# Optimization experiments

Measured on AMD Instinct MI355X. Metric: run time of the kernel, lower is better.

## Reference

```python
import jax, jax.numpy as jnp
import numpy as np

B, S, E, D = 4, 2048, 2048, 2048  # batch, seq (<= kvq_dim), embedding_dim, kvq_dim


def setup_inputs() -> dict:
    key = jax.random.key(0)
    kx, kk, kq, kv = jax.random.split(key, 4)
    x = jax.random.normal(kx, (B, S, E), dtype=jnp.float32)
    # torch nn.Linear weights are [out_features, in_features]
    Wk = jax.random.normal(kk, (D, E), dtype=jnp.float32) * 0.02
    Wq = jax.random.normal(kq, (D, E), dtype=jnp.float32) * 0.02
    Wv = jax.random.normal(kv, (D, E), dtype=jnp.float32) * 0.02
    return {"x": x, "Wk": Wk, "Wq": Wq, "Wv": Wv}


def reference(x, Wk, Wq, Wv):
    # Projections (Linear without bias): y = x @ W^T
    K = jnp.einsum("bse,de->bsd", x, Wk)
    Q = jnp.einsum("bse,de->bsd", x, Wq)
    V = jnp.einsum("bse,de->bsd", x, Wv)
    seq = x.shape[1]
    scores = jnp.einsum("bqd,bkd->bqk", Q, K)  # [B, S, S]
    causal = jnp.triu(jnp.ones((seq, seq), dtype=bool), k=1)
    masked = jnp.where(causal[None, :, :], -jnp.inf, scores)
    scale = K.shape[-1] ** 0.5  # -inf / scale stays -inf, matching the torch order
    attn = jax.nn.softmax(masked / scale, axis=-1)
    # dropout: reference evaluated in eval mode (identity)
    return jnp.einsum("bqk,bkd->bqd", attn, V)
```

## Files before the change

### kernel.cpp

```cpp
#include <hip/hip_runtime.h>
#include <hip/hip_bf16.h>
#include <stdint.h>


typedef unsigned short u16;
typedef unsigned int u32;
typedef __bf16 bf16x8 __attribute__((ext_vector_type(8)));
typedef float floatx4 __attribute__((ext_vector_type(4)));

#define DEVI __device__ __forceinline__

constexpr int Bn = 4, Sn = 2048, En = 2048, Dn = 2048;
constexpr int BM = 128, BN = 128, BK = 64;

DEVI u16 f2b(float f) {
  union { float f; u32 u; } v; v.f = f;
  u32 r = v.u + 0x7FFFu + ((v.u >> 16) & 1u);
  return (u16)(r >> 16);
}

DEVI void cp16(const u16* g, u16* l) {
  __builtin_amdgcn_global_load_lds(
      (const __attribute__((address_space(1))) void*)g,
      (__attribute__((address_space(3))) void*)l, 16, 0, 0);
}

__global__ __launch_bounds__(256)
void cvt_kernel(const float* __restrict__ src, u16* __restrict__ dst, int n) {
  int i = (blockIdx.x * 256 + threadIdx.x) * 8;
  if (i >= n) return;
  float4 a = *(const float4*)&src[i];
  float4 b = *(const float4*)&src[i + 4];
  *(ushort4*)&dst[i]     = make_ushort4(f2b(a.x), f2b(a.y), f2b(a.z), f2b(a.w));
  *(ushort4*)&dst[i + 4] = make_ushort4(f2b(b.x), f2b(b.y), f2b(b.z), f2b(b.w));
}

DEVI void gemm_core(const u16* __restrict__ A, const u16* __restrict__ Bt,
                    int lda, int ldb, int m0, int n0, int kEnd,
                    u16* As, u16* Bs, floatx4 acc[4][4]) {
  const int tid = threadIdx.x;
  const int lane = tid & 63;
  const int wave = tid >> 6;
  const int wm = (wave >> 1) * 64;
  const int wn = (wave & 1) * 64;
  const int quad = lane >> 4;
  const int l16 = lane & 15;
  const int sw = l16 & 7;

  int srow[4], sgl[4], sdst[4];
#pragma unroll
  for (int u = 0; u < 4; ++u) {
    int c0 = wave * 256 + u * 64;
    int c = c0 + lane;
    srow[u] = c >> 3;
    sgl[u] = (c & 7) ^ (srow[u] & 7);
    sdst[u] = c0 * 8;
  }

  for (int k0 = 0; k0 < kEnd; k0 += BK) {
#pragma unroll
    for (int u = 0; u < 4; ++u) {
      cp16(&A[(size_t)(m0 + srow[u]) * lda + k0 + sgl[u] * 8], &As[sdst[u]]);
      cp16(&Bt[(size_t)(n0 + srow[u]) * ldb + k0 + sgl[u] * 8], &Bs[sdst[u]]);
    }
    __syncthreads();
#pragma unroll
    for (int s = 0; s < 2; ++s) {
      const int gcol = ((s * 4 + quad) ^ sw) * 8;
      bf16x8 af[4], bfr[4];
#pragma unroll
      for (int i = 0; i < 4; ++i)
        af[i] = *(const bf16x8*)&As[(wm + i * 16 + l16) * 64 + gcol];
#pragma unroll
      for (int j = 0; j < 4; ++j)
        bfr[j] = *(const bf16x8*)&Bs[(wn + j * 16 + l16) * 64 + gcol];
#pragma unroll
      for (int i = 0; i < 4; ++i)
#pragma unroll
        for (int j = 0; j < 4; ++j)
          acc[i][j] = __builtin_amdgcn_mfma_f32_16x16x32_bf16(af[i], bfr[j], acc[i][j], 0, 0, 0);
    }
    __syncthreads();
  }
}

__global__ __launch_bounds__(256, 2)
void proj_kernel(const u16* __restrict__ x, const u16* __restrict__ Wq,
                 const u16* __restrict__ Wk, const u16* __restrict__ Wv,
                 u16* __restrict__ Q, u16* __restrict__ K, u16* __restrict__ Vt) {
  __shared__ __align__(16) u16 As[BM * 64], Bs[BN * 64];
  const int z = blockIdx.z;
  const u16* W = (z == 0) ? Wq : (z == 1) ? Wk : Wv;
  const int m0 = blockIdx.y * BM, n0 = blockIdx.x * BN;
  floatx4 acc[4][4] = {};
  gemm_core(x, W, En, En, m0, n0, En, As, Bs, acc);

  const int lane = threadIdx.x & 63, wave = threadIdx.x >> 6;
  const int wm = (wave >> 1) * 64, wn = (wave & 1) * 64;
  const int quad = lane >> 4, l16 = lane & 15;

  if (z < 2) {
    u16* dst = (z == 0) ? Q : K;
#pragma unroll
    for (int i = 0; i < 4; ++i) {
      int t0 = m0 + wm + i * 16 + quad * 4;
#pragma unroll
      for (int j = 0; j < 4; ++j) {
        int gn = n0 + wn + j * 16 + l16;
#pragma unroll
        for (int r = 0; r < 4; ++r)
          dst[(size_t)(t0 + r) * Dn + gn] = f2b(acc[i][j][r]);
      }
    }
  } else {
#pragma unroll
    for (int i = 0; i < 4; ++i) {
      int t0 = m0 + wm + i * 16 + quad * 4;
      int b = t0 >> 11, s0 = t0 & (Sn - 1);
#pragma unroll
      for (int j = 0; j < 4; ++j) {
        int gn = n0 + wn + j * 16 + l16;
        *(ushort4*)&Vt[((size_t)b * Dn + gn) * Sn + s0] =
            make_ushort4(f2b(acc[i][j][0]), f2b(acc[i][j][1]),
                         f2b(acc[i][j][2]), f2b(acc[i][j][3]));
      }
    }
  }
}

__global__ __launch_bounds__(256, 2)
void scores_kernel(const u16* __restrict__ Q, const u16* __restrict__ K,
                   float* __restrict__ Sc) {
  const int b = blockIdx.z;
  const int m0 = blockIdx.y * BM, n0 = blockIdx.x * BN;
  float* C = Sc + (size_t)b * Sn * Sn;
  if (n0 > m0 + (BM - 1)) {
    for (int idx = threadIdx.x; idx < BM * BN; idx += 256) {
      int r = idx >> 7, c = idx & (BN - 1);
      C[(size_t)(m0 + r) * Sn + n0 + c] = -1e30f;
    }
    return;
  }
  __shared__ __align__(16) u16 As[BM * 64], Bs[BN * 64];
  floatx4 acc[4][4] = {};
  gemm_core(Q + (size_t)b * Sn * Dn, K + (size_t)b * Sn * Dn, Dn, Dn, m0, n0, Dn,
            As, Bs, acc);

  const float inv_scale = 0.022097086912079608f;
  const int lane = threadIdx.x & 63, wave = threadIdx.x >> 6;
  const int wm = (wave >> 1) * 64, wn = (wave & 1) * 64;
  const int quad = lane >> 4, l16 = lane & 15;
#pragma unroll
  for (int i = 0; i < 4; ++i) {
    int gm0 = m0 + wm + i * 16 + quad * 4;
#pragma unroll
    for (int j = 0; j < 4; ++j) {
      int gn = n0 + wn + j * 16 + l16;
#pragma unroll
      for (int r = 0; r < 4; ++r) {
        float v = acc[i][j][r] * inv_scale;
        if (gn > gm0 + r) v = -1e30f;
        C[(size_t)(gm0 + r) * Sn + gn] = v;
      }
    }
  }
}

__global__ __launch_bounds__(256)
void softmax_kernel(float* __restrict__ Sc) {
  float* sr = Sc + (size_t)blockIdx.x * Sn;
  const int t = threadIdx.x;
  float4 v0 = ((const float4*)sr)[t];
  float4 v1 = ((const float4*)sr)[t + 256];
  float m = fmaxf(fmaxf(fmaxf(v0.x, v0.y), fmaxf(v0.z, v0.w)),
                  fmaxf(fmaxf(v1.x, v1.y), fmaxf(v1.z, v1.w)));
#pragma unroll
  for (int off = 32; off; off >>= 1) m = fmaxf(m, __shfl_xor(m, off));
  __shared__ float redm[4], reds[4];
  if ((t & 63) == 0) redm[t >> 6] = m;
  __syncthreads();
  m = fmaxf(fmaxf(redm[0], redm[1]), fmaxf(redm[2], redm[3]));

  float e[8];
  e[0] = __expf(v0.x - m); e[1] = __expf(v0.y - m);
  e[2] = __expf(v0.z - m); e[3] = __expf(v0.w - m);
  e[4] = __expf(v1.x - m); e[5] = __expf(v1.y - m);
  e[6] = __expf(v1.z - m); e[7] = __expf(v1.w - m);
  float s = ((e[0] + e[1]) + (e[2] + e[3])) + ((e[4] + e[5]) + (e[6] + e[7]));
#pragma unroll
  for (int off = 32; off; off >>= 1) s += __shfl_xor(s, off);
  if ((t & 63) == 0) reds[t >> 6] = s;
  __syncthreads();
  s = (reds[0] + reds[1]) + (reds[2] + reds[3]);
  float inv = 1.0f / s;

  u16* ar = (u16*)sr;
  *(ushort4*)&ar[t * 4] =
      make_ushort4(f2b(e[0] * inv), f2b(e[1] * inv), f2b(e[2] * inv), f2b(e[3] * inv));
  *(ushort4*)&ar[(t + 256) * 4] =
      make_ushort4(f2b(e[4] * inv), f2b(e[5] * inv), f2b(e[6] * inv), f2b(e[7] * inv));
}

__global__ __launch_bounds__(256, 2)
void pv_kernel(const float* __restrict__ Sc, const u16* __restrict__ Vt,
               float* __restrict__ out) {
  const int b = blockIdx.z;
  const int m0 = blockIdx.y * BM, n0 = blockIdx.x * BN;
  __shared__ __align__(16) u16 As[BM * 64], Bs[BN * 64];
  floatx4 acc[4][4] = {};
  const u16* P = (const u16*)(Sc + (size_t)b * Sn * Sn);
  gemm_core(P, Vt + (size_t)b * Dn * Sn, 2 * Sn, Sn, m0, n0, m0 + BM, As, Bs, acc);

  const int lane = threadIdx.x & 63, wave = threadIdx.x >> 6;
  const int wm = (wave >> 1) * 64, wn = (wave & 1) * 64;
  const int quad = lane >> 4, l16 = lane & 15;
  float* ob = out + (size_t)b * Sn * Dn;
#pragma unroll
  for (int i = 0; i < 4; ++i) {
    int gm0 = m0 + wm + i * 16 + quad * 4;
#pragma unroll
    for (int j = 0; j < 4; ++j) {
      int gn = n0 + wn + j * 16 + l16;
#pragma unroll
      for (int r = 0; r < 4; ++r)
        ob[(size_t)(gm0 + r) * Dn + gn] = acc[i][j][r];
    }
  }
}

extern "C" void kernel_launch(void* const* d_in, const int* in_sizes, int n_in,
                              void* d_out, int out_size, void* d_ws, size_t ws_size,
                              hipStream_t stream) {
  const float* x  = (const float*)d_in[0];
  const float* Wk = (const float*)d_in[1];
  const float* Wq = (const float*)d_in[2];
  const float* Wv = (const float*)d_in[3];
  float* out = (float*)d_out;

  dim3 blk(256);
  const int nW = Dn * En;
  const size_t MiB = 1ull << 20;

  if (ws_size >= 184 * MiB) {
    u16* Wqb = (u16*)d_ws;
    u16* Wkb = Wqb + (size_t)nW;
    u16* Wvb = Wkb + (size_t)nW;
    u16* xb  = Wvb + (size_t)nW;
    u16* Kall = xb + (size_t)Bn * Sn * En;
    u16* Vtall = Kall + (size_t)Bn * Sn * Dn;
    float* Sc = (float*)(Vtall + (size_t)Bn * Dn * Sn);
    u16* Qall = (u16*)out;

    cvt_kernel<<<nW / 2048, blk, 0, stream>>>(Wq, Wqb, nW);
    cvt_kernel<<<nW / 2048, blk, 0, stream>>>(Wk, Wkb, nW);
    cvt_kernel<<<nW / 2048, blk, 0, stream>>>(Wv, Wvb, nW);
    cvt_kernel<<<(Bn * Sn * En) / 2048, blk, 0, stream>>>(x, xb, Bn * Sn * En);
    proj_kernel<<<dim3(Dn / BN, (Bn * Sn) / BM, 3), blk, 0, stream>>>(
        xb, Wqb, Wkb, Wvb, Qall, Kall, Vtall);
    scores_kernel<<<dim3(Sn / BN, Sn / BM, Bn), blk, 0, stream>>>(Qall, Kall, Sc);
    softmax_kernel<<<dim3(Bn * Sn), blk, 0, stream>>>(Sc);
    pv_kernel<<<dim3(Dn / BN, Sn / BM, Bn), blk, 0, stream>>>(Sc, Vtall, out);
  } else {
    u16* Wqb = (u16*)d_ws;
    u16* Wkb = Wqb + (size_t)nW;
    u16* Wvb = Wkb + (size_t)nW;
    float* Sc = (float*)(Wvb + (size_t)nW);
    u16* xb  = (u16*)Sc;
    u16* Kb  = (u16*)(Sc + (size_t)Sn * Sn);
    u16* Vtb = Kb + (size_t)Sn * Dn;

    cvt_kernel<<<nW / 2048, blk, 0, stream>>>(Wq, Wqb, nW);
    cvt_kernel<<<nW / 2048, blk, 0, stream>>>(Wk, Wkb, nW);
    cvt_kernel<<<nW / 2048, blk, 0, stream>>>(Wv, Wvb, nW);
    for (int b = 0; b < Bn; ++b) {
      const float* xf = x + (size_t)b * Sn * En;
      float* outb = out + (size_t)b * Sn * Dn;
      u16* Qb = (u16*)outb;
      cvt_kernel<<<(Sn * En) / 2048, blk, 0, stream>>>(xf, xb, Sn * En);
      proj_kernel<<<dim3(Dn / BN, Sn / BM, 3), blk, 0, stream>>>(xb, Wqb, Wkb, Wvb,
                                                                 Qb, Kb, Vtb);
      scores_kernel<<<dim3(Sn / BN, Sn / BM, 1), blk, 0, stream>>>(Qb, Kb, Sc);
      softmax_kernel<<<dim3(Sn), blk, 0, stream>>>(Sc);
      pv_kernel<<<dim3(Dn / BN, Sn / BM, 1), blk, 0, stream>>>(Sc, Vtb, outb);
    }
  }
}
```

Baseline: 482.3 us.

## Replace GEMM core with 256x256 double-buffered, 8-wave pipelined MFMA mainloop

Replaces the 128x128 single-buffered GEMM core with a 256x256 tile over 8 waves, each computing a 128x64 sub-tile. The K loop is split into 32-wide half-stages that are double-buffered in 128 KB of LDS, with global-to-LDS async loads issued between MFMA phases and explicit vmcnt waits, barriers and setprio. This aims to hide load latency and raise arithmetic intensity for the projection, score and PV GEMMs. The cost is many fewer blocks per launch (worse tail and causal-skip granularity), heavy register and LDS use, and fragile manual synchronisation.

```diff
diff --git a/kernel.cpp b/kernel.cpp
--- a/kernel.cpp
+++ b/kernel.cpp
@@ -11,7 +11,6 @@
 #define DEVI __device__ __forceinline__
 
 constexpr int Bn = 4, Sn = 2048, En = 2048, Dn = 2048;
-constexpr int BM = 128, BN = 128, BK = 64;
 
 DEVI u16 f2b(float f) {
   union { float f; u32 u; } v; v.f = f;
@@ -35,130 +34,158 @@
   *(ushort4*)&dst[i + 4] = make_ushort4(f2b(b.x), f2b(b.y), f2b(b.z), f2b(b.w));
 }
 
-DEVI void gemm_core(const u16* __restrict__ A, const u16* __restrict__ Bt,
-                    int lda, int ldb, int m0, int n0, int kEnd,
-                    u16* As, u16* Bs, floatx4 acc[4][4]) {
+DEVI void gemm8(const u16* __restrict__ A, const u16* __restrict__ Bt,
+                int lda, int ldb, int m0, int n0, int kEnd, u16* lds,
+                floatx4 acc[8][4]) {
   const int tid = threadIdx.x;
-  const int lane = tid & 63;
-  const int wave = tid >> 6;
-  const int wm = (wave >> 1) * 64;
-  const int wn = (wave & 1) * 64;
-  const int quad = lane >> 4;
-  const int l16 = lane & 15;
-  const int sw = l16 & 7;
-
-  int srow[4], sgl[4], sdst[4];
-#pragma unroll
-  for (int u = 0; u < 4; ++u) {
-    int c0 = wave * 256 + u * 64;
+  const int wave = tid >> 6, lane = tid & 63;
+  const int wm = (wave >> 2) * 128, wn = (wave & 3) * 64;
+  const int quad = lane >> 4, l16 = lane & 15;
+  const int swe = (quad ^ ((l16 >> 1) & 3)) * 8;
+  const int nkt = kEnd >> 6;
+
+  int dstc[2];
+  const u16 *Asp[2], *Bsp[2];
+#pragma unroll
+  for (int q = 0; q < 2; ++q) {
+    int c0 = (q * 8 + wave) * 64;
     int c = c0 + lane;
-    srow[u] = c >> 3;
-    sgl[u] = (c & 7) ^ (srow[u] & 7);
-    sdst[u] = c0 * 8;
-  }
-
-  for (int k0 = 0; k0 < kEnd; k0 += BK) {
-#pragma unroll
-    for (int u = 0; u < 4; ++u) {
-      cp16(&A[(size_t)(m0 + srow[u]) * lda + k0 + sgl[u] * 8], &As[sdst[u]]);
-      cp16(&Bt[(size_t)(n0 + srow[u]) * ldb + k0 + sgl[u] * 8], &Bs[sdst[u]]);
-    }
-    __syncthreads();
-#pragma unroll
-    for (int s = 0; s < 2; ++s) {
-      const int gcol = ((s * 4 + quad) ^ sw) * 8;
-      bf16x8 af[4], bfr[4];
+    int sr = c >> 2;
+    int sg = ((c & 3) ^ ((sr >> 1) & 3)) * 8;
+    dstc[q] = c0 * 8;
+    Asp[q] = A + (size_t)(m0 + sr) * lda + sg;
+    Bsp[q] = Bt + (size_t)(n0 + sr) * ldb + sg;
+  }
+  const int rbA = (wm + l16) * 32 + swe;
+  const int rbB = 16384 + (wn + l16) * 32 + swe;
+
+#define STAGE(ktu, isB, sh)                                                  \
+  {                                                                          \
+    int kc = (ktu) < nkt ? (ktu) : (nkt - 1);  \
+    int ks = (kc << 6) + (sh) * 32;                                          \
+    int db = (((ktu) & 1) << 15) + (isB) * 16384 + (sh) * 8192;              \
+    cp16(((isB) ? Bsp[0] : Asp[0]) + ks, &lds[db + dstc[0]]);                \
+    cp16(((isB) ? Bsp[1] : Asp[1]) + ks, &lds[db + dstc[1]]);                \
+  }
+
+  STAGE(0, 0, 0); STAGE(0, 1, 0); STAGE(0, 0, 1); STAGE(0, 1, 1);
+  STAGE(1, 0, 0); STAGE(1, 1, 0);
+  asm volatile("s_waitcnt vmcnt(4)" ::: "memory");
+  __builtin_amdgcn_s_barrier();
+
+  for (int m = 0; m < nkt; ++m) {
+    const int bofs = (m & 1) << 15;
+    bf16x8 bf[4];
+#pragma unroll
+    for (int p = 0; p < 4; ++p) {
+      const int s = p >> 1, cm = p & 1;
+      bf16x8 af[4];
+      const int abase = bofs + s * 8192 + rbA + cm * 2048;
+#pragma unroll
+      for (int i = 0; i < 4; ++i) af[i] = *(const bf16x8*)&lds[abase + i * 512];
+      if (cm == 0) {
+        const int bbase = bofs + s * 8192 + rbB;
+#pragma unroll
+        for (int j = 0; j < 4; ++j) bf[j] = *(const bf16x8*)&lds[bbase + j * 512];
+      }
+      if (p == 0)      { STAGE(m + 1, 0, 1); }
+      else if (p == 1) { STAGE(m + 1, 1, 1); }
+      else if (p == 2) { STAGE(m + 2, 0, 0); }
+      else             { STAGE(m + 2, 1, 0); }
+      __builtin_amdgcn_s_barrier();
+      asm volatile("s_waitcnt lgkmcnt(0)" ::: "memory");
+      __builtin_amdgcn_sched_barrier(0);
+      __builtin_amdgcn_s_setprio(1);
 #pragma unroll
       for (int i = 0; i < 4; ++i)
-        af[i] = *(const bf16x8*)&As[(wm + i * 16 + l16) * 64 + gcol];
-#pragma unroll
-      for (int j = 0; j < 4; ++j)
-        bfr[j] = *(const bf16x8*)&Bs[(wn + j * 16 + l16) * 64 + gcol];
-#pragma unroll
-      for (int i = 0; i < 4; ++i)
 #pragma unroll
         for (int j = 0; j < 4; ++j)
-          acc[i][j] = __builtin_amdgcn_mfma_f32_16x16x32_bf16(af[i], bfr[j], acc[i][j], 0, 0, 0);
-    }
-    __syncthreads();
-  }
-}
-
-__global__ __launch_bounds__(256, 2)
+          acc[cm * 4 + i][j] = __builtin_amdgcn_mfma_f32_16x16x32_bf16(
+              af[i], bf[j], acc[cm * 4 + i][j], 0, 0, 0);
+      __builtin_amdgcn_s_setprio(0);
+      if (p == 3) asm volatile("s_waitcnt vmcnt(4)" ::: "memory");
+      __builtin_amdgcn_s_barrier();
+    }
+  }
+#undef STAGE
+}
+
+__global__ __launch_bounds__(512, 2)
 void proj_kernel(const u16* __restrict__ x, const u16* __restrict__ Wq,
                  const u16* __restrict__ Wk, const u16* __restrict__ Wv,
                  u16* __restrict__ Q, u16* __restrict__ K, u16* __restrict__ Vt) {
-  __shared__ __align__(16) u16 As[BM * 64], Bs[BN * 64];
+  __shared__ __align__(16) u16 lds[65536];
   const int z = blockIdx.z;
   const u16* W = (z == 0) ? Wq : (z == 1) ? Wk : Wv;
-  const int m0 = blockIdx.y * BM, n0 = blockIdx.x * BN;
-  floatx4 acc[4][4] = {};
-  gemm_core(x, W, En, En, m0, n0, En, As, Bs, acc);
+  const int m0 = blockIdx.y * 256, n0 = blockIdx.x * 256;
+  floatx4 acc[8][4] = {};
+  gemm8(x, W, En, En, m0, n0, En, lds, acc);
 
   const int lane = threadIdx.x & 63, wave = threadIdx.x >> 6;
-  const int wm = (wave >> 1) * 64, wn = (wave & 1) * 64;
+  const int wm = (wave >> 2) * 128, wn = (wave & 3) * 64;
   const int quad = lane >> 4, l16 = lane & 15;
 
   if (z < 2) {
     u16* dst = (z == 0) ? Q : K;
 #pragma unroll
-    for (int i = 0; i < 4; ++i) {
-      int t0 = m0 + wm + i * 16 + quad * 4;
+    for (int mi = 0; mi < 8; ++mi) {
+      int t0 = m0 + wm + mi * 16 + quad * 4;
 #pragma unroll
       for (int j = 0; j < 4; ++j) {
         int gn = n0 + wn + j * 16 + l16;
 #pragma unroll
         for (int r = 0; r < 4; ++r)
-          dst[(size_t)(t0 + r) * Dn + gn] = f2b(acc[i][j][r]);
+          dst[(size_t)(t0 + r) * Dn + gn] = f2b(acc[mi][j][r]);
       }
     }
   } else {
 #pragma unroll
-    for (int i = 0; i < 4; ++i) {
-      int t0 = m0 + wm + i * 16 + quad * 4;
+    for (int mi = 0; mi < 8; ++mi) {
+      int t0 = m0 + wm + mi * 16 + quad * 4;
       int b = t0 >> 11, s0 = t0 & (Sn - 1);
 #pragma unroll
       for (int j = 0; j < 4; ++j) {
         int gn = n0 + wn + j * 16 + l16;
         *(ushort4*)&Vt[((size_t)b * Dn + gn) * Sn + s0] =
-            make_ushort4(f2b(acc[i][j][0]), f2b(acc[i][j][1]),
-                         f2b(acc[i][j][2]), f2b(acc[i][j][3]));
+            make_ushort4(f2b(acc[mi][j][0]), f2b(acc[mi][j][1]),
+                         f2b(acc[mi][j][2]), f2b(acc[mi][j][3]));
       }
     }
   }
 }
 
-__global__ __launch_bounds__(256, 2)
+__global__ __launch_bounds__(512, 2)
 void scores_kernel(const u16* __restrict__ Q, const u16* __restrict__ K,
                    float* __restrict__ Sc) {
   const int b = blockIdx.z;
-  const int m0 = blockIdx.y * BM, n0 = blockIdx.x * BN;
+  const int m0 = blockIdx.y * 256, n0 = blockIdx.x * 256;
   float* C = Sc + (size_t)b * Sn * Sn;
-  if (n0 > m0 + (BM - 1)) {
-    for (int idx = threadIdx.x; idx < BM * BN; idx += 256) {
-      int r = idx >> 7, c = idx & (BN - 1);
-      C[(size_t)(m0 + r) * Sn + n0 + c] = -1e30f;
+  if (n0 > m0 + 255) {
+    const float4 f = make_float4(-1e30f, -1e30f, -1e30f, -1e30f);
+    for (int idx = threadIdx.x; idx < 256 * 64; idx += 512) {
+      int r = idx >> 6, c4 = (idx & 63) << 2;
+      *(float4*)&C[(size_t)(m0 + r) * Sn + n0 + c4] = f;
     }
     return;
   }
-  __shared__ __align__(16) u16 As[BM * 64], Bs[BN * 64];
-  floatx4 acc[4][4] = {};
-  gemm_core(Q + (size_t)b * Sn * Dn, K + (size_t)b * Sn * Dn, Dn, Dn, m0, n0, Dn,
-            As, Bs, acc);
+  __shared__ __align__(16) u16 lds[65536];
+  floatx4 acc[8][4] = {};
+  gemm8(Q + (size_t)b * Sn * Dn, K + (size_t)b * Sn * Dn, Dn, Dn, m0, n0, Dn,
+        lds, acc);
 
   const float inv_scale = 0.022097086912079608f;
   const int lane = threadIdx.x & 63, wave = threadIdx.x >> 6;
-  const int wm = (wave >> 1) * 64, wn = (wave & 1) * 64;
+  const int wm = (wave >> 2) * 128, wn = (wave & 3) * 64;
   const int quad = lane >> 4, l16 = lane & 15;
 #pragma unroll
-  for (int i = 0; i < 4; ++i) {
-    int gm0 = m0 + wm + i * 16 + quad * 4;
+  for (int mi = 0; mi < 8; ++mi) {
+    int gm0 = m0 + wm + mi * 16 + quad * 4;
 #pragma unroll
     for (int j = 0; j < 4; ++j) {
       int gn = n0 + wn + j * 16 + l16;
 #pragma unroll
       for (int r = 0; r < 4; ++r) {
-        float v = acc[i][j][r] * inv_scale;
+        float v = acc[mi][j][r] * inv_scale;
         if (gn > gm0 + r) v = -1e30f;
         C[(size_t)(gm0 + r) * Sn + gn] = v;
       }
@@ -201,29 +228,29 @@
       make_ushort4(f2b(e[4] * inv), f2b(e[5] * inv), f2b(e[6] * inv), f2b(e[7] * inv));
 }
 
-__global__ __launch_bounds__(256, 2)
+__global__ __launch_bounds__(512, 2)
 void pv_kernel(const float* __restrict__ Sc, const u16* __restrict__ Vt,
                float* __restrict__ out) {
   const int b = blockIdx.z;
-  const int m0 = blockIdx.y * BM, n0 = blockIdx.x * BN;
-  __shared__ __align__(16) u16 As[BM * 64], Bs[BN * 64];
-  floatx4 acc[4][4] = {};
+  const int m0 = blockIdx.y * 256, n0 = blockIdx.x * 256;
+  __shared__ __align__(16) u16 lds[65536];
+  floatx4 acc[8][4] = {};
   const u16* P = (const u16*)(Sc + (size_t)b * Sn * Sn);
-  gemm_core(P, Vt + (size_t)b * Dn * Sn, 2 * Sn, Sn, m0, n0, m0 + BM, As, Bs, acc);
+  gemm8(P, Vt + (size_t)b * Dn * Sn, 2 * Sn, Sn, m0, n0, m0 + 256, lds, acc);
 
   const int lane = threadIdx.x & 63, wave = threadIdx.x >> 6;
-  const int wm = (wave >> 1) * 64, wn = (wave & 1) * 64;
+  const int wm = (wave >> 2) * 128, wn = (wave & 3) * 64;
   const int quad = lane >> 4, l16 = lane & 15;
   float* ob = out + (size_t)b * Sn * Dn;
 #pragma unroll
-  for (int i = 0; i < 4; ++i) {
-    int gm0 = m0 + wm + i * 16 + quad * 4;
+  for (int mi = 0; mi < 8; ++mi) {
+    int gm0 = m0 + wm + mi * 16 + quad * 4;
 #pragma unroll
     for (int j = 0; j < 4; ++j) {
       int gn = n0 + wn + j * 16 + l16;
 #pragma unroll
       for (int r = 0; r < 4; ++r)
-        ob[(size_t)(gm0 + r) * Dn + gn] = acc[i][j][r];
+        ob[(size_t)(gm0 + r) * Dn + gn] = acc[mi][j][r];
     }
   }
 }
@@ -237,7 +264,7 @@
   const float* Wv = (const float*)d_in[3];
   float* out = (float*)d_out;
 
-  dim3 blk(256);
+  dim3 blk(256), blk5(512);
   const int nW = Dn * En;
   const size_t MiB = 1ull << 20;
 
@@ -255,11 +282,11 @@
     cvt_kernel<<<nW / 2048, blk, 0, stream>>>(Wk, Wkb, nW);
     cvt_kernel<<<nW / 2048, blk, 0, stream>>>(Wv, Wvb, nW);
     cvt_kernel<<<(Bn * Sn * En) / 2048, blk, 0, stream>>>(x, xb, Bn * Sn * En);
-    proj_kernel<<<dim3(Dn / BN, (Bn * Sn) / BM, 3), blk, 0, stream>>>(
+    proj_kernel<<<dim3(Dn / 256, (Bn * Sn) / 256, 3), blk5, 0, stream>>>(
         xb, Wqb, Wkb, Wvb, Qall, Kall, Vtall);
-    scores_kernel<<<dim3(Sn / BN, Sn / BM, Bn), blk, 0, stream>>>(Qall, Kall, Sc);
+    scores_kernel<<<dim3(Sn / 256, Sn / 256, Bn), blk5, 0, stream>>>(Qall, Kall, Sc);
     softmax_kernel<<<dim3(Bn * Sn), blk, 0, stream>>>(Sc);
-    pv_kernel<<<dim3(Dn / BN, Sn / BM, Bn), blk, 0, stream>>>(Sc, Vtall, out);
+    pv_kernel<<<dim3(Dn / 256, Sn / 256, Bn), blk5, 0, stream>>>(Sc, Vtall, out);
   } else {
     u16* Wqb = (u16*)d_ws;
     u16* Wkb = Wqb + (size_t)nW;
@@ -277,11 +304,11 @@
       float* outb = out + (size_t)b * Sn * Dn;
       u16* Qb = (u16*)outb;
       cvt_kernel<<<(Sn * En) / 2048, blk, 0, stream>>>(xf, xb, Sn * En);
-      proj_kernel<<<dim3(Dn / BN, Sn / BM, 3), blk, 0, stream>>>(xb, Wqb, Wkb, Wvb,
-                                                                 Qb, Kb, Vtb);
-      scores_kernel<<<dim3(Sn / BN, Sn / BM, 1), blk, 0, stream>>>(Qb, Kb, Sc);
+      proj_kernel<<<dim3(Dn / 256, Sn / 256, 3), blk5, 0, stream>>>(xb, Wqb, Wkb, Wvb,
+                                                                    Qb, Kb, Vtb);
+      scores_kernel<<<dim3(Sn / 256, Sn / 256, 1), blk5, 0, stream>>>(Qb, Kb, Sc);
       softmax_kernel<<<dim3(Sn), blk, 0, stream>>>(Sc);
-      pv_kernel<<<dim3(Dn / BN, Sn / BM, 1), blk, 0, stream>>>(Sc, Vtb, outb);
-    }
-  }
-}
+      pv_kernel<<<dim3(Dn / 256, Sn / 256, 1), blk5, 0, stream>>>(Sc, Vtb, outb);
+    }
+  }
+}
```

Measured after the change: 491.6 us. About the same (+1.9%).

## Skip masked score tiles, fuse bf16 conversions, and reverse PV tile order

Applied to the files above, without the earlier changes.

Scores blocks above the causal diagonal now return without writing -1e30 fill. Softmax instead synthesizes masked values in registers, reads only the columns up to the diagonal, and writes probabilities only up to the tile boundary that PV consumes. The four fp32-to-bf16 conversion launches are merged into one kernel. PV blocks are issued in reverse row order so the longest causal rows start first, which should improve load balance. This cuts memory traffic on the masked half of the score matrix, at the cost of more branching in softmax.

```diff
diff --git a/kernel.cpp b/kernel.cpp
--- a/kernel.cpp
+++ b/kernel.cpp
@@ -29,6 +29,24 @@
 void cvt_kernel(const float* __restrict__ src, u16* __restrict__ dst, int n) {
   int i = (blockIdx.x * 256 + threadIdx.x) * 8;
   if (i >= n) return;
+  float4 a = *(const float4*)&src[i];
+  float4 b = *(const float4*)&src[i + 4];
+  *(ushort4*)&dst[i]     = make_ushort4(f2b(a.x), f2b(a.y), f2b(a.z), f2b(a.w));
+  *(ushort4*)&dst[i + 4] = make_ushort4(f2b(b.x), f2b(b.y), f2b(b.z), f2b(b.w));
+}
+
+__global__ __launch_bounds__(256)
+void cvt4_kernel(const float* __restrict__ x, const float* __restrict__ Wq,
+                 const float* __restrict__ Wk, const float* __restrict__ Wv,
+                 u16* __restrict__ xb, u16* __restrict__ Wqb,
+                 u16* __restrict__ Wkb, u16* __restrict__ Wvb) {
+  int bi = blockIdx.x;
+  const float* src; u16* dst; int base;
+  if (bi < 2048)      { src = Wq; dst = Wqb; base = bi; }
+  else if (bi < 4096) { src = Wk; dst = Wkb; base = bi - 2048; }
+  else if (bi < 6144) { src = Wv; dst = Wvb; base = bi - 4096; }
+  else                { src = x;  dst = xb;  base = bi - 6144; }
+  int i = (base * 256 + threadIdx.x) * 8;
   float4 a = *(const float4*)&src[i];
   float4 b = *(const float4*)&src[i + 4];
   *(ushort4*)&dst[i]     = make_ushort4(f2b(a.x), f2b(a.y), f2b(a.z), f2b(a.w));
@@ -133,14 +151,8 @@
                    float* __restrict__ Sc) {
   const int b = blockIdx.z;
   const int m0 = blockIdx.y * BM, n0 = blockIdx.x * BN;
+  if (n0 > m0 + (BM - 1)) return;
   float* C = Sc + (size_t)b * Sn * Sn;
-  if (n0 > m0 + (BM - 1)) {
-    for (int idx = threadIdx.x; idx < BM * BN; idx += 256) {
-      int r = idx >> 7, c = idx & (BN - 1);
-      C[(size_t)(m0 + r) * Sn + n0 + c] = -1e30f;
-    }
-    return;
-  }
   __shared__ __align__(16) u16 As[BM * 64], Bs[BN * 64];
   floatx4 acc[4][4] = {};
   gemm_core(Q + (size_t)b * Sn * Dn, K + (size_t)b * Sn * Dn, Dn, Dn, m0, n0, Dn,
@@ -168,10 +180,19 @@
 
 __global__ __launch_bounds__(256)
 void softmax_kernel(float* __restrict__ Sc) {
+  const int row = blockIdx.x & (Sn - 1);
   float* sr = Sc + (size_t)blockIdx.x * Sn;
   const int t = threadIdx.x;
-  float4 v0 = ((const float4*)sr)[t];
-  float4 v1 = ((const float4*)sr)[t + 256];
+  const int c0 = t * 4, c1 = 1024 + t * 4;
+  float4 v0 = make_float4(-1e30f, -1e30f, -1e30f, -1e30f), v1 = v0;
+  if (c0 <= row) v0 = ((const float4*)sr)[t];
+  if (c1 <= row) v1 = ((const float4*)sr)[t + 256];
+  if (c0 + 1 > row) v0.y = -1e30f;
+  if (c0 + 2 > row) v0.z = -1e30f;
+  if (c0 + 3 > row) v0.w = -1e30f;
+  if (c1 + 1 > row) v1.y = -1e30f;
+  if (c1 + 2 > row) v1.z = -1e30f;
+  if (c1 + 3 > row) v1.w = -1e30f;
   float m = fmaxf(fmaxf(fmaxf(v0.x, v0.y), fmaxf(v0.z, v0.w)),
                   fmaxf(fmaxf(v1.x, v1.y), fmaxf(v1.z, v1.w)));
 #pragma unroll
@@ -194,18 +215,22 @@
   s = (reds[0] + reds[1]) + (reds[2] + reds[3]);
   float inv = 1.0f / s;
 
+  const int wlim = (row & ~(BM - 1)) + BM;
   u16* ar = (u16*)sr;
-  *(ushort4*)&ar[t * 4] =
-      make_ushort4(f2b(e[0] * inv), f2b(e[1] * inv), f2b(e[2] * inv), f2b(e[3] * inv));
-  *(ushort4*)&ar[(t + 256) * 4] =
-      make_ushort4(f2b(e[4] * inv), f2b(e[5] * inv), f2b(e[6] * inv), f2b(e[7] * inv));
+  if (c0 < wlim)
+    *(ushort4*)&ar[t * 4] =
+        make_ushort4(f2b(e[0] * inv), f2b(e[1] * inv), f2b(e[2] * inv), f2b(e[3] * inv));
+  if (c1 < wlim)
+    *(ushort4*)&ar[(t + 256) * 4] =
+        make_ushort4(f2b(e[4] * inv), f2b(e[5] * inv), f2b(e[6] * inv), f2b(e[7] * inv));
 }
 
 __global__ __launch_bounds__(256, 2)
 void pv_kernel(const float* __restrict__ Sc, const u16* __restrict__ Vt,
                float* __restrict__ out) {
   const int b = blockIdx.z;
-  const int m0 = blockIdx.y * BM, n0 = blockIdx.x * BN;
+  const int m0 = ((int)gridDim.y - 1 - (int)blockIdx.y) * BM;
+  const int n0 = blockIdx.x * BN;
   __shared__ __align__(16) u16 As[BM * 64], Bs[BN * 64];
   floatx4 acc[4][4] = {};
   const u16* P = (const u16*)(Sc + (size_t)b * Sn * Sn);
@@ -251,10 +276,8 @@
     float* Sc = (float*)(Vtall + (size_t)Bn * Dn * Sn);
     u16* Qall = (u16*)out;
 
-    cvt_kernel<<<nW / 2048, blk, 0, stream>>>(Wq, Wqb, nW);
-    cvt_kernel<<<nW / 2048, blk, 0, stream>>>(Wk, Wkb, nW);
-    cvt_kernel<<<nW / 2048, blk, 0, stream>>>(Wv, Wvb, nW);
-    cvt_kernel<<<(Bn * Sn * En) / 2048, blk, 0, stream>>>(x, xb, Bn * Sn * En);
+    cvt4_kernel<<<3 * (nW / 2048) + (Bn * Sn * En) / 2048, blk, 0, stream>>>(
+        x, Wq, Wk, Wv, xb, Wqb, Wkb, Wvb);
     proj_kernel<<<dim3(Dn / BN, (Bn * Sn) / BM, 3), blk, 0, stream>>>(
         xb, Wqb, Wkb, Wvb, Qall, Kall, Vtall);
     scores_kernel<<<dim3(Sn / BN, Sn / BM, Bn), blk, 0, stream>>>(Qall, Kall, Sc);
```

New measurement: 477.9 us. About the same (-0.9%).
